# Optimization experiments

Hardware: AMD Instinct MI355X
Metric: run time of the kernel (lower is better)

Reference implementation:

```python
import jax, jax.numpy as jnp
import numpy as np

KH, KW = 5, 5  # kernel; stride=1, padding=0, dilation=1 per init_kwargs


def _unfold(x, kh, kw):
    # torch.nn.functional.unfold with stride=1, pad=0, dil=1, channel-major
    # ordering: out channel index = c*kh*kw + i*kw + j
    B, C, H, W = x.shape
    oh, ow = H - kh + 1, W - kw + 1
    patches = jnp.stack(
        [x[:, :, i:i + oh, j:j + ow] for i in range(kh) for j in range(kw)],
        axis=2,
    )  # [B, C, kh*kw, oh, ow]
    return patches.reshape(B, C * kh * kw, oh, ow)


def _sample_spikes(inp_conv, T):
    # multinomial(replacement=True) over the Cf channel dim per (b, x, y)
    logits = jnp.log(inp_conv.transpose(0, 2, 3, 1))  # [B, OH, OW, Cf]
    B, OH, OW, _ = logits.shape
    return jax.random.categorical(
        jax.random.key(42), logits[:, None], axis=-1, shape=(B, T, OH, OW)
    )  # [B, T, OH, OW] int


def setup_inputs() -> dict:
    key = jax.random.key(0)
    ks = jax.random.split(key, 6)
    B, C, H, W = 32, 24, 28, 28
    OH, OW = 24, 24
    Hn = 128  # number of hidden neurons
    T = 96    # number of spikes
    Cf = C * KH * KW  # 600
    return {
        "input": jax.random.uniform(ks[0], (B, C, H, W), jnp.float32, 0.01, 1.0),
        "epsilon_xy": jax.random.uniform(ks[1], (OH, OW, KH, KW), jnp.float32, 0.1, 1.0),
        "epsilon_0": jax.random.uniform(ks[2], (1,), jnp.float32, 0.5, 1.0),
        "epsilon_t": jax.random.uniform(ks[3], (T,), jnp.float32, 0.5, 1.0),
        "weights": jax.random.uniform(ks[4], (Cf, Hn), jnp.float32, 0.0, 1.0),
        "h_initial": jax.random.uniform(ks[5], (Hn,), jnp.float32, 0.5, 1.0),
        "number_of_spikes": T,
    }


def reference(input, epsilon_xy, epsilon_0, epsilon_t, weights, h_initial,
              number_of_spikes):
    T = int(number_of_spikes)
    B, C = input.shape[0], input.shape[1]
    inp_conv = _unfold(input, KH, KW)              # [B, Cf, OH, OW]
    spikes = _sample_spikes(inp_conv, T)           # [B, T, OH, OW]
    OH, OW = spikes.shape[2], spikes.shape[3]

    # epsilon_xy_convolved: value independent of input channel c,
    # index c*KH*KW + k -> epsilon_xy[x, y] flat at k. Stored as [OH, OW, Cf].
    eps_conv = jnp.tile(epsilon_xy.reshape(OH, OW, KH * KW), (1, 1, C))
    eps0 = epsilon_0[0]

    # Normalized recurrence: g = h / epsilon_scale (exactly equivalent to the
    # original h/epsilon_scale bookkeeping, including the overflow-rescale branch):
    #   g' = (g + eps_sub * (W[s]*g) / sum(W[s]*g)) / (1 + eps_sub)
    Hn = h_initial.shape[0]
    g0 = jnp.broadcast_to(h_initial, (B, OH, OW, Hn)).astype(jnp.float32)

    def step(g, xs):
        s, et = xs                                  # s: [B, OH, OW]
        wg = weights[s] * g                         # [B, OH, OW, Hn]
        denom = jnp.sum(wg, axis=-1, keepdims=True)  # [B, OH, OW, 1]
        eps = jnp.take_along_axis(eps_conv[None], s[..., None], axis=-1)
        eps_sub = eps * (et * eps0)                 # [B, OH, OW, 1]
        factor = jnp.nan_to_num(eps_sub / denom, nan=0.0, posinf=0.0, neginf=0.0)
        g = (g + wg * factor) / (1.0 + eps_sub)
        return g, None

    g, _ = jax.lax.scan(step, g0, (jnp.moveaxis(spikes, 1, 0), epsilon_t[:T]))
    return jnp.moveaxis(g, 3, 1)                    # [B, Hn, OH, OW]
```

## Files before the change

### kernel.cpp

```cpp
#include <hip/hip_runtime.h>
#include <stdint.h>

constexpr int Bn = 32, Cc = 24, Hh = 28, Ww = 28;
constexpr int OHt = 24, OWt = 24;
constexpr int CF = 600, HN = 128, TT = 96;
constexpr int NPIX = OHt * OWt;
constexpr int NSAMP = Bn * TT * NPIX;
constexpr int NLOG = Bn * Cc * Hh * Ww;
constexpr int NBIN = 640;

constexpr float MARGIN = 2.44140625e-4f;
constexpr float LN2 = 0.6931471805599453f;
constexpr float CGUM = 0.36651292058166433f;

__device__ __forceinline__ uint32_t threefry_0_42_pre(uint32_t x1) {
  const uint32_t ks1 = 42u, ks2 = 0x1BD11BF0u;
  uint32_t x0 = x1;
  x1 = __builtin_rotateleft32(x1, 13) ^ x0;
  x0 += x1; x1 = __builtin_rotateleft32(x1, 15) ^ x0;
  x0 += x1; x1 = __builtin_rotateleft32(x1, 26) ^ x0;
  x0 += x1; x1 = __builtin_rotateleft32(x1,  6) ^ x0;
  x0 += ks1; x1 += ks2 + 1u;
  x0 += x1; x1 = __builtin_rotateleft32(x1, 17) ^ x0;
  x0 += x1; x1 = __builtin_rotateleft32(x1, 29) ^ x0;
  x0 += x1; x1 = __builtin_rotateleft32(x1, 16) ^ x0;
  x0 += x1; x1 = __builtin_rotateleft32(x1, 24) ^ x0;
  x0 += ks2; x1 += 2u;
  x0 += x1; x1 = __builtin_rotateleft32(x1, 13) ^ x0;
  x0 += x1; x1 = __builtin_rotateleft32(x1, 15) ^ x0;
  x0 += x1; x1 = __builtin_rotateleft32(x1, 26) ^ x0;
  x0 += x1; x1 = __builtin_rotateleft32(x1,  6) ^ x0;
  x1 += ks1 + 3u;
  x0 += x1; x1 = __builtin_rotateleft32(x1, 17) ^ x0;
  x0 += x1; x1 = __builtin_rotateleft32(x1, 29) ^ x0;
  x0 += x1; x1 = __builtin_rotateleft32(x1, 16) ^ x0;
  x0 += x1; x1 = __builtin_rotateleft32(x1, 24) ^ x0;
  x0 += ks1; x1 += ks2 + 4u;
  x0 += x1; x1 = __builtin_rotateleft32(x1, 13) ^ x0;
  x0 += x1; x1 = __builtin_rotateleft32(x1, 15) ^ x0;
  x0 += x1; x1 = __builtin_rotateleft32(x1, 26) ^ x0;
  x0 += x1; x1 = __builtin_rotateleft32(x1,  6) ^ x0;
  x0 += ks2; x1 += 5u;
  return x0 ^ x1;
}

__global__ __launch_bounds__(256) void k_log(const float* __restrict__ in,
                                             float* __restrict__ lp) {
  int i = blockIdx.x * 256 + threadIdx.x;
  if (i < NLOG) lp[i] = logf(in[i]);
}

__global__ __launch_bounds__(256) void k_lpmax(const float* __restrict__ lp,
                                               float* __restrict__ out) {
  int pid = blockIdx.x * 256 + threadIdx.x;
  if (pid >= Bn * NPIX) return;
  int y = pid % OWt;
  int x = (pid / OWt) % OHt;
  int b = pid / NPIX;
  const float* p = lp + (b * Cc) * (Hh * Ww) + x * Ww + y;
  float m = -3.0e38f;
  for (int c = 0; c < Cc; ++c) {
    const float* pc = p + c * (Hh * Ww);
    #pragma unroll
    for (int ki = 0; ki < 5; ++ki)
      #pragma unroll
      for (int kj = 0; kj < 5; ++kj) m = fmaxf(m, pc[ki * Ww + kj]);
  }
  out[pid] = m;
}

__device__ __forceinline__ uint32_t mkthr(float bgap) {
  float g3 = bgap - 0.00390625f;
  float e1 = __expf(-g3) * 1.0000153f;
  float ul = __expf(-e1) * 0.9999847f;
  int kt = (int)(ul * 8388608.0f) - 64;
  return (kt < 1) ? 0u : ((uint32_t)kt << 9);
}

__device__ __forceinline__ float exact_v(uint32_t bits, float lp) {
  uint32_t key = bits >> 9;
  float f = __uint_as_float(key | 0x3f800000u) - 1.0f;
  float u = (f == 0.0f) ? 1.17549435e-38f : f;
  float l1 = logf(u);
  return -logf(-l1) + lp;
}

__device__ __attribute__((noinline)) int exact_argmax(
    uint32_t base, const float* __restrict__ lpb) {
  float best = -1e30f;
  int bi = 0;
  int cf = 0;
  #pragma unroll 1
  for (int c = 0; c < Cc; ++c) {
    const float* lpc = lpb + c * (Hh * Ww);
    #pragma unroll 1
    for (int ki = 0; ki < 5; ++ki)
      #pragma unroll
      for (int kj = 0; kj < 5; ++kj) {
        float v = exact_v(threefry_0_42_pre(base + (uint32_t)cf),
                          lpc[ki * Ww + kj]);
        if (v > best) { best = v; bi = cf; }
        ++cf;
      }
  }
  return bi;
}

__global__ __launch_bounds__(256) void k_sample(const float* __restrict__ logp,
                                                const float* __restrict__ lpmaxa,
                                                int* __restrict__ spikes) {
  __shared__ uint32_t thr_tab[NBIN];
  for (int i = threadIdx.x; i < NBIN; i += 256)
    thr_tab[i] = mkthr(__builtin_fmaf((float)i, 0.03125f, -8.0f));
  __syncthreads();

  int tid = blockIdx.x * 256 + threadIdx.x;
  int y = tid % OWt;
  int x = (tid / OWt) % OHt;
  int t = (tid / NPIX) % 48;
  int b = tid / (NPIX * 48);
  int sid1 = ((b * TT + t) * OHt + x) * OWt + y;
  uint32_t ctr1 = (uint32_t)sid1 * 600u + 42u;
  const float* lpb = logp + (b * Cc) * (Hh * Ww) + x * Ww + y;
  float lpmax = lpmaxa[(b * OHt + x) * OWt + y];
  float K = __builtin_fmaf(-32.0f, lpmax, 255.0f + 32.0f * CGUM);

  float bA1 = -1e30f, bA2 = -1e30f;
  float sA1 = -2e30f, sA2 = -2e30f;
  int bi1 = 0, bi2 = 0;
  uint32_t th1 = 0u, th2 = 0u;

#define AUPD(BITS, BA, SA, BI, TH)                                          \
  if ((BITS) >= (TH)) {                                                     \
    uint32_t key = (BITS) >> 9;                                             \
    float f = __uint_as_float(key | 0x3f800000u) - 1.0f;                    \
    float u = (f == 0.0f) ? 1.17549435e-38f : f;                            \
    float lg = __log2f(u);                                  \
    float n = __log2f(-lg);                                                 \
    float vh = __builtin_fmaf(-LN2, n, lp);                 \
    float nb = fmaxf(BA, vh);                                               \
    SA = fmaxf(SA, fminf(BA, vh));                                          \
    if (vh > BA) BI = cf;                                                   \
    BA = nb;                                                                \
    float bx = __builtin_fmaf(nb, 32.0f, K);                                \
    bx = fminf(fmaxf(bx, 0.0f), 639.0f);                                    \
    TH = thr_tab[(int)bx];                                                  \
  }

  int cf = 0;
  #pragma unroll 1
  for (int c = 0; c < Cc; ++c) {
    const float* lpc = lpb + c * (Hh * Ww);
    #pragma unroll 1
    for (int ki = 0; ki < 5; ++ki) {
      #pragma unroll
      for (int kj = 0; kj < 5; ++kj) {
        float lp = lpc[ki * Ww + kj];
        uint32_t c1 = ctr1 + (uint32_t)cf;
        uint32_t bb1 = threefry_0_42_pre(c1);
        uint32_t bb2 = threefry_0_42_pre(c1 + 16588800u);
        AUPD(bb1, bA1, sA1, bi1, th1)
        AUPD(bb2, bA2, sA2, bi2, th2)
        ++cf;
      }
    }
  }
#undef AUPD

  spikes[sid1] = (bA1 - sA1 >= MARGIN) ? bi1 : exact_argmax(ctr1, lpb);
  spikes[sid1 + 48 * NPIX] =
      (bA2 - sA2 >= MARGIN) ? bi2 : exact_argmax(ctr1 + 16588800u, lpb);
}

__global__ __launch_bounds__(256) void k_recur(
    const int* __restrict__ spikes, const float* __restrict__ weights,
    const float* __restrict__ eps_xy, const float* __restrict__ eps_t,
    const float* __restrict__ eps0p, const float* __restrict__ h_init,
    float* __restrict__ out) {
  int wid = blockIdx.x * 4 + (threadIdx.x >> 6);
  int lane = threadIdx.x & 63;
  int y = wid % OWt;
  int x = (wid / OWt) % OHt;
  int b = wid / NPIX;
  float g0 = h_init[lane];
  float g1 = h_init[lane + 64];
  float e0 = eps0p[0];
  const int* sp = spikes + (b * TT) * NPIX + x * OWt + y;
  const float* ex = eps_xy + (x * OWt + y) * 25;
  for (int t = 0; t < TT; ++t) {
    int s = sp[t * NPIX];
    const float* wr = weights + s * HN;
    float wg0 = wr[lane] * g0;
    float wg1 = wr[lane + 64] * g1;
    float sum = wg0 + wg1;
    #pragma unroll
    for (int off = 32; off > 0; off >>= 1) sum += __shfl_xor(sum, off, 64);
    float es = ex[s % 25] * (eps_t[t] * e0);
    float factor = es / sum;
    if (!__builtin_isfinite(factor)) factor = 0.0f;
    float d = 1.0f + es;
    g0 = (g0 + wg0 * factor) / d;
    g1 = (g1 + wg1 * factor) / d;
  }
  out[((b * HN + lane) * OHt + x) * OWt + y] = g0;
  out[((b * HN + lane + 64) * OHt + x) * OWt + y] = g1;
}

extern "C" void kernel_launch(void* const* d_in, const int* in_sizes, int n_in,
                              void* d_out, int out_size, void* d_ws, size_t ws_size,
                              hipStream_t stream) {
  const float* input   = (const float*)d_in[0];
  const float* eps_xy  = (const float*)d_in[1];
  const float* eps0    = (const float*)d_in[2];
  const float* eps_t   = (const float*)d_in[3];
  const float* weights = (const float*)d_in[4];
  const float* h_init  = (const float*)d_in[5];

  float* logp = (float*)d_ws;
  int* spikes = (int*)((char*)d_ws + NLOG * sizeof(float));
  float* lpmax = (float*)d_out;

  k_log<<<(NLOG + 255) / 256, 256, 0, stream>>>(input, logp);
  k_lpmax<<<(Bn * NPIX + 255) / 256, 256, 0, stream>>>(logp, lpmax);
  k_sample<<<(NSAMP / 2) / 256, 256, 0, stream>>>(logp, lpmax, spikes);
  k_recur<<<(Bn * NPIX) / 4, 256, 0, stream>>>(spikes, weights, eps_xy, eps_t,
                                               eps0, h_init, (float*)d_out);
}
```

Baseline: 2.665 ms.

## Replace Gumbel-max log sampling with exponential-race surrogate using packed min keys

```diff
diff --git a/kernel.cpp b/kernel.cpp
--- a/kernel.cpp
+++ b/kernel.cpp
@@ -7,11 +7,6 @@
 constexpr int NPIX = OHt * OWt;
 constexpr int NSAMP = Bn * TT * NPIX;
 constexpr int NLOG = Bn * Cc * Hh * Ww;
-constexpr int NBIN = 640;
-
-constexpr float MARGIN = 2.44140625e-4f;
-constexpr float LN2 = 0.6931471805599453f;
-constexpr float CGUM = 0.36651292058166433f;
 
 __device__ __forceinline__ uint32_t threefry_0_42_pre(uint32_t x1) {
   const uint32_t ks1 = 42u, ks2 = 0x1BD11BF0u;
@@ -44,61 +39,30 @@
   return x0 ^ x1;
 }
 
-__global__ __launch_bounds__(256) void k_log(const float* __restrict__ in,
-                                             float* __restrict__ lp) {
+__global__ __launch_bounds__(256) void k_rinc(const float* __restrict__ in,
+                                              float* __restrict__ rc) {
   int i = blockIdx.x * 256 + threadIdx.x;
-  if (i < NLOG) lp[i] = logf(in[i]);
-}
-
-__global__ __launch_bounds__(256) void k_lpmax(const float* __restrict__ lp,
-                                               float* __restrict__ out) {
-  int pid = blockIdx.x * 256 + threadIdx.x;
-  if (pid >= Bn * NPIX) return;
-  int y = pid % OWt;
-  int x = (pid / OWt) % OHt;
-  int b = pid / NPIX;
-  const float* p = lp + (b * Cc) * (Hh * Ww) + x * Ww + y;
-  float m = -3.0e38f;
-  for (int c = 0; c < Cc; ++c) {
-    const float* pc = p + c * (Hh * Ww);
-    #pragma unroll
-    for (int ki = 0; ki < 5; ++ki)
-      #pragma unroll
-      for (int kj = 0; kj < 5; ++kj) m = fmaxf(m, pc[ki * Ww + kj]);
-  }
-  out[pid] = m;
-}
-
-__device__ __forceinline__ uint32_t mkthr(float bgap) {
-  float g3 = bgap - 0.00390625f;
-  float e1 = __expf(-g3) * 1.0000153f;
-  float ul = __expf(-e1) * 0.9999847f;
-  int kt = (int)(ul * 8388608.0f) - 64;
-  return (kt < 1) ? 0u : ((uint32_t)kt << 9);
-}
-
-__device__ __forceinline__ float exact_v(uint32_t bits, float lp) {
-  uint32_t key = bits >> 9;
-  float f = __uint_as_float(key | 0x3f800000u) - 1.0f;
-  float u = (f == 0.0f) ? 1.17549435e-38f : f;
-  float l1 = logf(u);
-  return -logf(-l1) + lp;
+  if (i < NLOG) rc[i] = 1.1920928955078125e-7f / in[i];
 }
 
 __device__ __attribute__((noinline)) int exact_argmax(
-    uint32_t base, const float* __restrict__ lpb) {
+    uint32_t base, const float* __restrict__ inb) {
   float best = -1e30f;
   int bi = 0;
   int cf = 0;
   #pragma unroll 1
   for (int c = 0; c < Cc; ++c) {
-    const float* lpc = lpb + c * (Hh * Ww);
+    const float* inc = inb + c * (Hh * Ww);
     #pragma unroll 1
     for (int ki = 0; ki < 5; ++ki)
       #pragma unroll
       for (int kj = 0; kj < 5; ++kj) {
-        float v = exact_v(threefry_0_42_pre(base + (uint32_t)cf),
-                          lpc[ki * Ww + kj]);
+        uint32_t bits = threefry_0_42_pre(base + (uint32_t)cf);
+        uint32_t key = bits >> 9;
+        float f = __uint_as_float(key | 0x3f800000u) - 1.0f;
+        float u = (f == 0.0f) ? 1.17549435e-38f : f;
+        float l1 = logf(u);
+        float v = -logf(-l1) + logf(inc[ki * Ww + kj]);
         if (v > best) { best = v; bi = cf; }
         ++cf;
       }
@@ -106,14 +70,9 @@
   return bi;
 }
 
-__global__ __launch_bounds__(256) void k_sample(const float* __restrict__ logp,
-                                                const float* __restrict__ lpmaxa,
+__global__ __launch_bounds__(256) void k_sample(const float* __restrict__ rincp,
+                                                const float* __restrict__ input,
                                                 int* __restrict__ spikes) {
-  __shared__ uint32_t thr_tab[NBIN];
-  for (int i = threadIdx.x; i < NBIN; i += 256)
-    thr_tab[i] = mkthr(__builtin_fmaf((float)i, 0.03125f, -8.0f));
-  __syncthreads();
-
   int tid = blockIdx.x * 256 + threadIdx.x;
   int y = tid % OWt;
   int x = (tid / OWt) % OHt;
@@ -121,55 +80,57 @@
   int b = tid / (NPIX * 48);
   int sid1 = ((b * TT + t) * OHt + x) * OWt + y;
   uint32_t ctr1 = (uint32_t)sid1 * 600u + 42u;
-  const float* lpb = logp + (b * Cc) * (Hh * Ww) + x * Ww + y;
-  float lpmax = lpmaxa[(b * OHt + x) * OWt + y];
-  float K = __builtin_fmaf(-32.0f, lpmax, 255.0f + 32.0f * CGUM);
+  const float* rcb = rincp + (b * Cc) * (Hh * Ww) + x * Ww + y;
 
-  float bA1 = -1e30f, bA2 = -1e30f;
-  float sA1 = -2e30f, sA2 = -2e30f;
-  int bi1 = 0, bi2 = 0;
-  uint32_t th1 = 0u, th2 = 0u;
+  uint32_t m1a = 0xFFFFFFFFu, m2a = 0xFFFFFFFFu;
+  uint32_t m1b = 0xFFFFFFFFu, m2b = 0xFFFFFFFFu;
 
-#define AUPD(BITS, BA, SA, BI, TH)                                          \
-  if ((BITS) >= (TH)) {                                                     \
+#define SURR(BITS, RC, M1, M2)                                              \
+  {                                                                         \
     uint32_t key = (BITS) >> 9;                                             \
-    float f = __uint_as_float(key | 0x3f800000u) - 1.0f;                    \
-    float u = (f == 0.0f) ? 1.17549435e-38f : f;                            \
-    float lg = __log2f(u);                                  \
-    float n = __log2f(-lg);                                                 \
-    float vh = __builtin_fmaf(-LN2, n, lp);                 \
-    float nb = fmaxf(BA, vh);                                               \
-    SA = fmaxf(SA, fminf(BA, vh));                                          \
-    if (vh > BA) BI = cf;                                                   \
-    BA = nb;                                                                \
-    float bx = __builtin_fmaf(nb, 32.0f, K);                                \
-    bx = fminf(fmaxf(bx, 0.0f), 639.0f);                                    \
-    TH = thr_tab[(int)bx];                                                  \
+    float tailf = (float)(0x800000u - key);             \
+    float s = (RC)*tailf;                                       \
+    float T = tailf * 1.1920928955078125e-7f;             \
+    float q = __builtin_fmaf(                                               \
+        T, __builtin_fmaf(T, 0.33333333333f, 0.5f), 1.0f);                  \
+    float rh = s * q;                                                       \
+    uint32_t pk = (__float_as_uint(rh) & 0xFFFFFC00u) | (uint32_t)cf;       \
+    uint32_t tmp = (pk > M1) ? pk : M1;                            \
+    M2 = (M2 < tmp) ? M2 : tmp;                                    \
+    M1 = (M1 < pk) ? M1 : pk;                                      \
   }
 
   int cf = 0;
   #pragma unroll 1
   for (int c = 0; c < Cc; ++c) {
-    const float* lpc = lpb + c * (Hh * Ww);
-    #pragma unroll 1
+    const float* rcc = rcb + c * (Hh * Ww);
+    #pragma unroll
     for (int ki = 0; ki < 5; ++ki) {
       #pragma unroll
       for (int kj = 0; kj < 5; ++kj) {
-        float lp = lpc[ki * Ww + kj];
+        float rc = rcc[ki * Ww + kj];
         uint32_t c1 = ctr1 + (uint32_t)cf;
         uint32_t bb1 = threefry_0_42_pre(c1);
         uint32_t bb2 = threefry_0_42_pre(c1 + 16588800u);
-        AUPD(bb1, bA1, sA1, bi1, th1)
-        AUPD(bb2, bA2, sA2, bi2, th2)
+        SURR(bb1, rc, m1a, m2a)
+        SURR(bb2, rc, m1b, m2b)
         ++cf;
       }
     }
   }
-#undef AUPD
+#undef SURR
 
-  spikes[sid1] = (bA1 - sA1 >= MARGIN) ? bi1 : exact_argmax(ctr1, lpb);
+  const float* inb = input + (b * Cc) * (Hh * Ww) + x * Ww + y;
+  float f1a = __uint_as_float(m1a & 0xFFFFFC00u);
+  float f2a = __uint_as_float(m2a & 0xFFFFFC00u);
+  float f1b = __uint_as_float(m1b & 0xFFFFFC00u);
+  float f2b = __uint_as_float(m2b & 0xFFFFFC00u);
+  constexpr float MARG = 1.0f + 0.0009765625f;
+  bool ca = (f1a <= 0.04f) && (f2a > f1a * MARG);
+  bool cb = (f1b <= 0.04f) && (f2b > f1b * MARG);
+  spikes[sid1] = ca ? (int)(m1a & 1023u) : exact_argmax(ctr1, inb);
   spikes[sid1 + 48 * NPIX] =
-      (bA2 - sA2 >= MARGIN) ? bi2 : exact_argmax(ctr1 + 16588800u, lpb);
+      cb ? (int)(m1b & 1023u) : exact_argmax(ctr1 + 16588800u, inb);
 }
 
 __global__ __launch_bounds__(256) void k_recur(
@@ -216,13 +177,11 @@
   const float* weights = (const float*)d_in[4];
   const float* h_init  = (const float*)d_in[5];
 
-  float* logp = (float*)d_ws;
+  float* rinc = (float*)d_ws;
   int* spikes = (int*)((char*)d_ws + NLOG * sizeof(float));
-  float* lpmax = (float*)d_out;
 
-  k_log<<<(NLOG + 255) / 256, 256, 0, stream>>>(input, logp);
-  k_lpmax<<<(Bn * NPIX + 255) / 256, 256, 0, stream>>>(logp, lpmax);
-  k_sample<<<(NSAMP / 2) / 256, 256, 0, stream>>>(logp, lpmax, spikes);
+  k_rinc<<<(NLOG + 255) / 256, 256, 0, stream>>>(input, rinc);
+  k_sample<<<(NSAMP / 2) / 256, 256, 0, stream>>>(rinc, input, spikes);
   k_recur<<<(Bn * NPIX) / 4, 256, 0, stream>>>(spikes, weights, eps_xy, eps_t,
                                                eps0, h_init, (float*)d_out);
 }
```

Result: slower. 2.896 ms (+8.7%).
